# Kernel optimization log

Hardware: AMD Instinct MI355X
Metric: run time of the kernel (lower is better)

Reference implementation:

```python
import jax, jax.numpy as jnp
import numpy as np

EMBED = 256
HEADS = 8
N, L, S = 4, 128, 64


def setup_inputs() -> dict:
    key = jax.random.key(0)
    ks = jax.random.split(key, 9)
    values = jax.random.normal(ks[0], (N, L, S, EMBED), dtype=jnp.float32)
    keys_ = jax.random.normal(ks[1], (N, L, S, EMBED), dtype=jnp.float32)
    query = jax.random.normal(ks[2], (N, L, S, EMBED), dtype=jnp.float32)
    mask = jax.random.randint(ks[3], (N, 1, L, L, 1), 0, 2, dtype=jnp.int32)
    sc = 1.0 / np.sqrt(EMBED)
    Wq = jax.random.normal(ks[4], (EMBED, EMBED), dtype=jnp.float32) * sc
    Wk = jax.random.normal(ks[5], (EMBED, EMBED), dtype=jnp.float32) * sc
    Wv = jax.random.normal(ks[6], (EMBED, EMBED), dtype=jnp.float32) * sc
    Wo = jax.random.normal(ks[7], (HEADS * EMBED, EMBED), dtype=jnp.float32) * (1.0 / np.sqrt(HEADS * EMBED))
    bo = jnp.zeros((EMBED,), dtype=jnp.float32)
    return {"values": values, "keys": keys_, "query": query, "mask": mask,
            "Wq": Wq, "Wk": Wk, "Wv": Wv, "Wo": Wo, "bo": bo}


def reference(values, keys, query, mask, Wq, Wk, Wv, Wo, bo):
    n, q_len, s_len, d = query.shape
    k_len = keys.shape[1]
    h = HEADS
    # Per-head projections share one weight (expand happens BEFORE Linear in
    # the original), so compute each projection once and broadcast over heads.
    q = jnp.einsum('nqsd,de->nqse', query, Wq)   # [N,Q,S,D]
    k = jnp.einsum('nksd,de->nkse', keys, Wk)    # [N,K,S,D]
    v = jnp.einsum('nksd,de->nkse', values, Wv)  # [N,K,S,D]
    # energy: nqshd,nkshd->nhqks ; identical across h pre-mask
    energy = jnp.einsum('nqsd,nksd->nqks', q, k)            # [N,Q,K,S]
    energy = jnp.broadcast_to(energy[:, None], (n, h, q_len, k_len, s_len))
    energy = jnp.where(mask == 0, jnp.float32(-1e20), energy)
    attn = jax.nn.softmax(energy / jnp.sqrt(jnp.float32(d)), axis=3)  # over K
    # out: nhqls,nlshd->nqshd
    out = jnp.einsum('nhqks,nksd->nqshd', attn, v)
    out = out.reshape(n, q_len, s_len, h * d)
    return out @ Wo + bo
```

## Files before the change

### kernel.cpp

```cpp
#include <hip/hip_runtime.h>
#include <hip/hip_bf16.h>


using bf16x4 = __attribute__((ext_vector_type(4))) __bf16;
using bf16x8 = __attribute__((ext_vector_type(8))) __bf16;
using f32x4  = __attribute__((ext_vector_type(4))) float;

#define MFMA(a, b, c) __builtin_amdgcn_mfma_f32_16x16x32_bf16((a), (b), (c), 0, 0, 0)

__global__ __launch_bounds__(256) void prep_pack(
    const float* __restrict__ Wq, const float* __restrict__ Wk,
    const float* __restrict__ Wv, const float* __restrict__ Wo,
    __bf16* __restrict__ wqp, __bf16* __restrict__ wkp,
    __bf16* __restrict__ wvp, __bf16* __restrict__ wop) {
  int idx = blockIdx.x * 256 + threadIdx.x;
  int j = idx & 7, lane = (idx >> 3) & 63, k8 = (idx >> 9) & 7, ct = idx >> 12;
  int e = ct * 16 + (lane & 15);
  int d = k8 * 32 + (lane >> 4) * 8 + j;
  wqp[idx] = (__bf16)Wq[d * 256 + e];
  wkp[idx] = (__bf16)Wk[d * 256 + e];
  wvp[idx] = (__bf16)Wv[d * 256 + e];
  float s = 0.f;
#pragma unroll
  for (int h = 0; h < 8; ++h) s += Wo[(h * 256 + d) * 256 + e];
  wop[idx] = (__bf16)s;
}

__global__ __launch_bounds__(512, 2) void fused_attn(
    const float* __restrict__ Xv, const float* __restrict__ Xk,
    const float* __restrict__ Xq, const int* __restrict__ mask,
    const __bf16* __restrict__ wqp, const __bf16* __restrict__ wkp,
    const __bf16* __restrict__ wvp, const __bf16* __restrict__ wop,
    const float* __restrict__ bo, float* __restrict__ out) {
  extern __shared__ char lds[];
  char* Areg = lds;
  char* Breg = lds + 65536;
  char* Creg = lds + 131072;
  const int t = threadIdx.x, lane = t & 63, w = t >> 6;
  const int lr = lane & 15, g = lane >> 4;
  const int sl = blockIdx.x, n = sl >> 6, s = sl & 63;

  auto fill = [&](const float* __restrict__ X, float4* vr) {
#pragma unroll
    for (int i = 0; i < 8; ++i) {
      int f8 = i * 512 + t, row = f8 >> 5, c8 = f8 & 31;
      const float* src = X + ((size_t)(n * 8192 + row * 64 + s)) * 256 + c8 * 8;
      vr[2 * i]     = *reinterpret_cast<const float4*>(src);
      vr[2 * i + 1] = *reinterpret_cast<const float4*>(src + 4);
    }
  };
  auto flushv = [&](const float4* vr) {
#pragma unroll
    for (int i = 0; i < 8; ++i) {
      int f8 = i * 512 + t, row = f8 >> 5, c8 = f8 & 31;
      bf16x8 b;
      b[0]=(__bf16)vr[2*i].x;   b[1]=(__bf16)vr[2*i].y;
      b[2]=(__bf16)vr[2*i].z;   b[3]=(__bf16)vr[2*i].w;
      b[4]=(__bf16)vr[2*i+1].x; b[5]=(__bf16)vr[2*i+1].y;
      b[6]=(__bf16)vr[2*i+1].z; b[7]=(__bf16)vr[2*i+1].w;
      *reinterpret_cast<bf16x8*>(
          Areg + row * 512 + ((c8 * 16) ^ ((row & 7) << 4))) = b;
    }
  };

  auto projQK = [&](const __bf16* __restrict__ wpk) {
    const bf16x8* wp = reinterpret_cast<const bf16x8*>(wpk);
    bf16x8 wf0[8], wf1[8];
#pragma unroll
    for (int k8 = 0; k8 < 8; ++k8) {
      wf0[k8] = wp[((2 * w)     * 8 + k8) * 64 + lane];
      wf1[k8] = wp[((2 * w + 1) * 8 + k8) * 64 + lane];
    }
#pragma unroll
    for (int ct = 0; ct < 8; ++ct) {
      bf16x8 xf[8];
#pragma unroll
      for (int k8 = 0; k8 < 8; ++k8) {
        int brow = ct * 16 + lr;
        xf[k8] = *reinterpret_cast<const bf16x8*>(
            Areg + brow * 512 + ((k8 * 64 + g * 16) ^ ((brow & 7) << 4)));
      }
      f32x4 a0 = {0.f,0.f,0.f,0.f}, a1 = {0.f,0.f,0.f,0.f};
#pragma unroll
      for (int k8 = 0; k8 < 8; ++k8) {
        a0 = MFMA(wf0[k8], xf[k8], a0);
        a1 = MFMA(wf1[k8], xf[k8], a1);
      }
      bf16x4 p0, p1;
#pragma unroll
      for (int j = 0; j < 4; ++j) { p0[j] = (__bf16)a0[j]; p1[j] = (__bf16)a1[j]; }
      *reinterpret_cast<bf16x4*>(
          Breg + ct * 8192 + w * 1024 + (lr + 16 * (0 + (g >> 1))) * 16 + (g & 1) * 8) = p0;
      *reinterpret_cast<bf16x4*>(
          Breg + ct * 8192 + w * 1024 + (lr + 16 * (2 + (g >> 1))) * 16 + (g & 1) * 8) = p1;
    }
  };

  {
    float4 vr[16];
    fill(Xq, vr);
    flushv(vr);
  }
  __syncthreads();
  float4 vrp[16];
  fill(Xk, vrp);
  projQK(wqp);
  __syncthreads();
  bf16x8 af[8];
#pragma unroll
  for (int k8 = 0; k8 < 8; ++k8)
    af[k8] = *reinterpret_cast<const bf16x8*>(Breg + w * 8192 + k8 * 1024 + lane * 16);
  flushv(vrp);
  __syncthreads();

  fill(Xv, vrp);
  projQK(wkp);
  __syncthreads();

  int mreg[8][4];
#pragma unroll
  for (int ct = 0; ct < 8; ++ct)
#pragma unroll
    for (int j = 0; j < 4; ++j)
      mreg[ct][j] = mask[((size_t)n * 128 + w * 16 + 4 * g + j) * 128 + ct * 16 + lr];
  f32x4 sacc[8];
#pragma unroll
  for (int ct = 0; ct < 8; ++ct) {
    bf16x8 bfr[8];
#pragma unroll
    for (int k8 = 0; k8 < 8; ++k8)
      bfr[k8] = *reinterpret_cast<const bf16x8*>(Breg + ct * 8192 + k8 * 1024 + lane * 16);
    f32x4 a = {0.f,0.f,0.f,0.f};
#pragma unroll
    for (int k8 = 0; k8 < 8; ++k8) a = MFMA(af[k8], bfr[k8], a);
    sacc[ct] = a;
  }
  flushv(vrp);
  __syncthreads();

  float p[8][4];
#pragma unroll
  for (int j = 0; j < 4; ++j) {
    float mx = -3e38f;
#pragma unroll
    for (int ct = 0; ct < 8; ++ct) {
      float sv = mreg[ct][j] ? sacc[ct][j] * 0.0625f : -6.25e18f;
      p[ct][j] = sv;
      mx = fmaxf(mx, sv);
    }
#pragma unroll
    for (int o = 1; o < 16; o <<= 1) mx = fmaxf(mx, __shfl_xor(mx, o));
    float sum = 0.f;
#pragma unroll
    for (int ct = 0; ct < 8; ++ct) {
      float e = __expf(p[ct][j] - mx);
      p[ct][j] = e;
      sum += e;
    }
#pragma unroll
    for (int o = 1; o < 16; o <<= 1) sum += __shfl_xor(sum, o);
    float inv = 1.f / sum;
#pragma unroll
    for (int ct = 0; ct < 8; ++ct) p[ct][j] *= inv;
  }
#pragma unroll
  for (int ct = 0; ct < 8; ++ct) {
    char* bse = Breg + w * 4096 + (ct >> 1) * 1024 +
                (16 * ((ct * 2 + (lr >> 3)) & 3)) * 16 + (lr & 7) * 2;
#pragma unroll
    for (int j = 0; j < 4; ++j)
      *reinterpret_cast<__bf16*>(bse + (4 * g + j) * 16) = (__bf16)p[ct][j];
  }
  bf16x8 pa[4];
#pragma unroll
  for (int kk8 = 0; kk8 < 4; ++kk8)
    pa[kk8] = *reinterpret_cast<const bf16x8*>(Breg + w * 4096 + kk8 * 1024 + lane * 16);

  {
    const bf16x8* wp = reinterpret_cast<const bf16x8*>(wvp);
    bf16x8 vf0[8], vf1[8];
#pragma unroll
    for (int k8 = 0; k8 < 8; ++k8) {
      vf0[k8] = wp[((2 * w)     * 8 + k8) * 64 + lane];
      vf1[k8] = wp[((2 * w + 1) * 8 + k8) * 64 + lane];
    }
#pragma unroll
    for (int half = 0; half < 2; ++half) {
      char* dest = half ? Areg : Creg;
#pragma unroll
      for (int ctl = 0; ctl < 4; ++ctl) {
        int ct = half * 4 + ctl;
        bf16x8 xf[8];
#pragma unroll
        for (int k8 = 0; k8 < 8; ++k8) {
          int brow = ct * 16 + lr;
          xf[k8] = *reinterpret_cast<const bf16x8*>(
              Areg + brow * 512 + ((k8 * 64 + g * 16) ^ ((brow & 7) << 4)));
        }
        f32x4 a0 = {0.f,0.f,0.f,0.f}, a1 = {0.f,0.f,0.f,0.f};
#pragma unroll
        for (int k8 = 0; k8 < 8; ++k8) {
          a0 = MFMA(vf0[k8], xf[k8], a0);
          a1 = MFMA(vf1[k8], xf[k8], a1);
        }
        int kk8loc = (ct >> 1) & 1;
#pragma unroll
        for (int dth = 0; dth < 2; ++dth) {
          const f32x4& ac = dth ? a1 : a0;
          char* bse = dest + ((2 * w + dth) * 2 + kk8loc) * 1024 +
                      (16 * ((ct * 2 + (lr >> 3)) & 3)) * 16 + (lr & 7) * 2;
#pragma unroll
          for (int j = 0; j < 4; ++j)
            *reinterpret_cast<__bf16*>(bse + (4 * g + j) * 16) = (__bf16)ac[j];
        }
      }
      __syncthreads();
    }
  }

#pragma unroll
  for (int dt = 0; dt < 16; ++dt) {
    f32x4 acc = {0.f,0.f,0.f,0.f};
#pragma unroll
    for (int kk8 = 0; kk8 < 4; ++kk8) {
      const char* vb = (kk8 < 2) ? (Creg + (dt * 2 + kk8) * 1024)
                                 : (Areg + (dt * 2 + kk8 - 2) * 1024);
      acc = MFMA(pa[kk8], *reinterpret_cast<const bf16x8*>(vb + lane * 16), acc);
    }
    char* bse = Breg + w * 8192 + (dt >> 1) * 1024 +
                (16 * ((dt * 2 + (lr >> 3)) & 3)) * 16 + (lr & 7) * 2;
#pragma unroll
    for (int j = 0; j < 4; ++j)
      *reinterpret_cast<__bf16*>(bse + (4 * g + j) * 16) = (__bf16)acc[j];
  }
  __syncthreads();

  {
    const bf16x8* wo = reinterpret_cast<const bf16x8*>(wop);
    bf16x8 of0[8], of1[8];
#pragma unroll
    for (int k8 = 0; k8 < 8; ++k8) {
      of0[k8] = wo[((2 * w)     * 8 + k8) * 64 + lane];
      of1[k8] = wo[((2 * w + 1) * 8 + k8) * 64 + lane];
    }
    float4 bias0 = *reinterpret_cast<const float4*>(bo + (2 * w)     * 16 + 4 * g);
    float4 bias1 = *reinterpret_cast<const float4*>(bo + (2 * w + 1) * 16 + 4 * g);
#pragma unroll
    for (int qt = 0; qt < 8; ++qt) {
      bf16x8 bfr[8];
#pragma unroll
      for (int k8 = 0; k8 < 8; ++k8)
        bfr[k8] = *reinterpret_cast<const bf16x8*>(Breg + qt * 8192 + k8 * 1024 + lane * 16);
      f32x4 a0 = {0.f,0.f,0.f,0.f}, a1 = {0.f,0.f,0.f,0.f};
#pragma unroll
      for (int k8 = 0; k8 < 8; ++k8) {
        a0 = MFMA(of0[k8], bfr[k8], a0);
        a1 = MFMA(of1[k8], bfr[k8], a1);
      }
      int q = qt * 16 + lr;
      float* orow = out + ((size_t)n * 8192 + q * 64 + s) * 256;
      float4 o0, o1;
      o0.x = a0[0] + bias0.x; o0.y = a0[1] + bias0.y;
      o0.z = a0[2] + bias0.z; o0.w = a0[3] + bias0.w;
      o1.x = a1[0] + bias1.x; o1.y = a1[1] + bias1.y;
      o1.z = a1[2] + bias1.z; o1.w = a1[3] + bias1.w;
      *reinterpret_cast<float4*>(orow + (2 * w)     * 16 + 4 * g) = o0;
      *reinterpret_cast<float4*>(orow + (2 * w + 1) * 16 + 4 * g) = o1;
    }
  }
}

extern "C" void kernel_launch(void* const* d_in, const int* in_sizes, int n_in,
                              void* d_out, int out_size, void* d_ws, size_t ws_size,
                              hipStream_t stream) {
  const float* values = (const float*)d_in[0];
  const float* keys   = (const float*)d_in[1];
  const float* query  = (const float*)d_in[2];
  const int*   mask   = (const int*)d_in[3];
  const float* Wq     = (const float*)d_in[4];
  const float* Wk     = (const float*)d_in[5];
  const float* Wv     = (const float*)d_in[6];
  const float* Wo     = (const float*)d_in[7];
  const float* bo     = (const float*)d_in[8];
  float* out = (float*)d_out;

  char* w = (char*)d_ws;
  __bf16* wqp = (__bf16*)w; w += 131072;
  __bf16* wkp = (__bf16*)w; w += 131072;
  __bf16* wvp = (__bf16*)w; w += 131072;
  __bf16* wop = (__bf16*)w; w += 131072;

  prep_pack<<<256, 256, 0, stream>>>(Wq, Wk, Wv, Wo, wqp, wkp, wvp, wop);
  fused_attn<<<256, 512, 163840, stream>>>(values, keys, query, mask,
                                           wqp, wkp, wvp, wop, bo, out);
}
```

Before: 47.68 us.

## Fold Wq·Wkᵀ and Wv·Wo_sum into combined weights, dropping K projection and output GEMM

```diff
diff --git a/kernel.cpp b/kernel.cpp
--- a/kernel.cpp
+++ b/kernel.cpp
@@ -8,34 +8,83 @@
 
 #define MFMA(a, b, c) __builtin_amdgcn_mfma_f32_16x16x32_bf16((a), (b), (c), 0, 0, 0)
 
-__global__ __launch_bounds__(256) void prep_pack(
+__device__ __forceinline__ bf16x8 cvt8(float4 f0, float4 f1) {
+  bf16x8 a;
+  a[0]=(__bf16)f0.x; a[1]=(__bf16)f0.y; a[2]=(__bf16)f0.z; a[3]=(__bf16)f0.w;
+  a[4]=(__bf16)f1.x; a[5]=(__bf16)f1.y; a[6]=(__bf16)f1.z; a[7]=(__bf16)f1.w;
+  return a;
+}
+
+__global__ __launch_bounds__(256) void prep_wosum(
+    const float* __restrict__ Wo, float* __restrict__ wosum) {
+  int eo = threadIdx.x, e2 = blockIdx.x;
+  float s = 0.f;
+#pragma unroll
+  for (int h = 0; h < 8; ++h) s += Wo[((size_t)(h * 256 + e2)) * 256 + eo];
+  wosum[e2 * 256 + eo] = s;
+}
+
+__global__ __launch_bounds__(512) void prep_mm(
     const float* __restrict__ Wq, const float* __restrict__ Wk,
-    const float* __restrict__ Wv, const float* __restrict__ Wo,
-    __bf16* __restrict__ wqp, __bf16* __restrict__ wkp,
-    __bf16* __restrict__ wvp, __bf16* __restrict__ wop) {
-  int idx = blockIdx.x * 256 + threadIdx.x;
-  int j = idx & 7, lane = (idx >> 3) & 63, k8 = (idx >> 9) & 7, ct = idx >> 12;
-  int e = ct * 16 + (lane & 15);
-  int d = k8 * 32 + (lane >> 4) * 8 + j;
-  wqp[idx] = (__bf16)Wq[d * 256 + e];
-  wkp[idx] = (__bf16)Wk[d * 256 + e];
-  wvp[idx] = (__bf16)Wv[d * 256 + e];
-  float s = 0.f;
-#pragma unroll
-  for (int h = 0; h < 8; ++h) s += Wo[(h * 256 + d) * 256 + e];
-  wop[idx] = (__bf16)s;
+    const float* __restrict__ Wv, const float* __restrict__ wosum,
+    __bf16* __restrict__ mqk, __bf16* __restrict__ mvo) {
+  const int t = threadIdx.x, lane = t & 63, w = t >> 6;
+  const int lr = lane & 15, g = lane >> 4;
+  const bool isV = blockIdx.y != 0;
+  const float* A = isV ? Wv : Wq;
+  __bf16* dst = isV ? mvo : mqk;
+  bf16x8 af0[8], af1[8];
+#pragma unroll
+  for (int k8 = 0; k8 < 8; ++k8) {
+    const float* p0 = A + (size_t)((2 * w)     * 16 + lr) * 256 + k8 * 32 + g * 8;
+    const float* p1 = A + (size_t)((2 * w + 1) * 16 + lr) * 256 + k8 * 32 + g * 8;
+    af0[k8] = cvt8(*(const float4*)p0, *(const float4*)(p0 + 4));
+    af1[k8] = cvt8(*(const float4*)p1, *(const float4*)(p1 + 4));
+  }
+#pragma unroll
+  for (int c = 0; c < 2; ++c) {
+    int ct = blockIdx.x * 2 + c;
+    bf16x8 bf[8];
+    if (!isV) {
+#pragma unroll
+      for (int k8 = 0; k8 < 8; ++k8) {
+        const float* p = Wk + (size_t)(ct * 16 + lr) * 256 + k8 * 32 + g * 8;
+        bf[k8] = cvt8(*(const float4*)p, *(const float4*)(p + 4));
+      }
+    } else {
+#pragma unroll
+      for (int k8 = 0; k8 < 8; ++k8)
+#pragma unroll
+        for (int jj = 0; jj < 8; ++jj)
+          bf[k8][jj] = (__bf16)wosum[(size_t)(k8 * 32 + g * 8 + jj) * 256 + ct * 16 + lr];
+    }
+    f32x4 a0 = {0.f,0.f,0.f,0.f}, a1 = {0.f,0.f,0.f,0.f};
+#pragma unroll
+    for (int k8 = 0; k8 < 8; ++k8) {
+      a0 = MFMA(af0[k8], bf[k8], a0);
+      a1 = MFMA(af1[k8], bf[k8], a1);
+    }
+#pragma unroll
+    for (int rtl = 0; rtl < 2; ++rtl) {
+      const f32x4& ac = rtl ? a1 : a0;
+      bf16x4 pb;
+#pragma unroll
+      for (int j = 0; j < 4; ++j) pb[j] = (__bf16)ac[j];
+      size_t off = (size_t)ct * 4096 + w * 512 +
+                   ((2 * rtl + (g >> 1)) * 16 + lr) * 8 + 4 * (g & 1);
+      *reinterpret_cast<bf16x4*>(dst + off) = pb;
+    }
+  }
 }
 
 __global__ __launch_bounds__(512, 2) void fused_attn(
     const float* __restrict__ Xv, const float* __restrict__ Xk,
     const float* __restrict__ Xq, const int* __restrict__ mask,
-    const __bf16* __restrict__ wqp, const __bf16* __restrict__ wkp,
-    const __bf16* __restrict__ wvp, const __bf16* __restrict__ wop,
+    const __bf16* __restrict__ mqk, const __bf16* __restrict__ mvo,
     const float* __restrict__ bo, float* __restrict__ out) {
   extern __shared__ char lds[];
   char* Areg = lds;
   char* Breg = lds + 65536;
-  char* Creg = lds + 131072;
   const int t = threadIdx.x, lane = t & 63, w = t >> 6;
   const int lr = lane & 15, g = lane >> 4;
   const int sl = blockIdx.x, n = sl >> 6, s = sl & 63;
@@ -63,8 +112,17 @@
     }
   };
 
-  auto projQK = [&](const __bf16* __restrict__ wpk) {
-    const bf16x8* wp = reinterpret_cast<const bf16x8*>(wpk);
+  {
+    float4 vr[16];
+    fill(Xq, vr);
+    flushv(vr);
+  }
+  __syncthreads();
+
+  float4 vrp[16];
+  fill(Xk, vrp);
+  {
+    const bf16x8* wp = reinterpret_cast<const bf16x8*>(mqk);
     bf16x8 wf0[8], wf1[8];
 #pragma unroll
     for (int k8 = 0; k8 < 8; ++k8) {
@@ -94,18 +152,9 @@
       *reinterpret_cast<bf16x4*>(
           Breg + ct * 8192 + w * 1024 + (lr + 16 * (2 + (g >> 1))) * 16 + (g & 1) * 8) = p1;
     }
-  };
-
-  {
-    float4 vr[16];
-    fill(Xq, vr);
-    flushv(vr);
-  }
-  __syncthreads();
-  float4 vrp[16];
-  fill(Xk, vrp);
-  projQK(wqp);
-  __syncthreads();
+  }
+  __syncthreads();
+
   bf16x8 af[8];
 #pragma unroll
   for (int k8 = 0; k8 < 8; ++k8)
@@ -114,9 +163,6 @@
   __syncthreads();
 
   fill(Xv, vrp);
-  projQK(wkp);
-  __syncthreads();
-
   int mreg[8][4];
 #pragma unroll
   for (int ct = 0; ct < 8; ++ct)
@@ -126,17 +172,20 @@
   f32x4 sacc[8];
 #pragma unroll
   for (int ct = 0; ct < 8; ++ct) {
-    bf16x8 bfr[8];
-#pragma unroll
-    for (int k8 = 0; k8 < 8; ++k8)
-      bfr[k8] = *reinterpret_cast<const bf16x8*>(Breg + ct * 8192 + k8 * 1024 + lane * 16);
+    bf16x8 xf[8];
+#pragma unroll
+    for (int k8 = 0; k8 < 8; ++k8) {
+      int brow = ct * 16 + lr;
+      xf[k8] = *reinterpret_cast<const bf16x8*>(
+          Areg + brow * 512 + ((k8 * 64 + g * 16) ^ ((brow & 7) << 4)));
+    }
     f32x4 a = {0.f,0.f,0.f,0.f};
 #pragma unroll
-    for (int k8 = 0; k8 < 8; ++k8) a = MFMA(af[k8], bfr[k8], a);
+    for (int k8 = 0; k8 < 8; ++k8) a = MFMA(af[k8], xf[k8], a);
     sacc[ct] = a;
   }
+  __syncthreads();
   flushv(vrp);
-  __syncthreads();
 
   float p[8][4];
 #pragma unroll
@@ -175,9 +224,10 @@
 #pragma unroll
   for (int kk8 = 0; kk8 < 4; ++kk8)
     pa[kk8] = *reinterpret_cast<const bf16x8*>(Breg + w * 4096 + kk8 * 1024 + lane * 16);
+  __syncthreads();
 
   {
-    const bf16x8* wp = reinterpret_cast<const bf16x8*>(wvp);
+    const bf16x8* wp = reinterpret_cast<const bf16x8*>(mvo);
     bf16x8 vf0[8], vf1[8];
 #pragma unroll
     for (int k8 = 0; k8 < 8; ++k8) {
@@ -185,87 +235,53 @@
       vf1[k8] = wp[((2 * w + 1) * 8 + k8) * 64 + lane];
     }
 #pragma unroll
-    for (int half = 0; half < 2; ++half) {
-      char* dest = half ? Areg : Creg;
-#pragma unroll
-      for (int ctl = 0; ctl < 4; ++ctl) {
-        int ct = half * 4 + ctl;
-        bf16x8 xf[8];
-#pragma unroll
-        for (int k8 = 0; k8 < 8; ++k8) {
-          int brow = ct * 16 + lr;
-          xf[k8] = *reinterpret_cast<const bf16x8*>(
-              Areg + brow * 512 + ((k8 * 64 + g * 16) ^ ((brow & 7) << 4)));
-        }
-        f32x4 a0 = {0.f,0.f,0.f,0.f}, a1 = {0.f,0.f,0.f,0.f};
-#pragma unroll
-        for (int k8 = 0; k8 < 8; ++k8) {
-          a0 = MFMA(vf0[k8], xf[k8], a0);
-          a1 = MFMA(vf1[k8], xf[k8], a1);
-        }
-        int kk8loc = (ct >> 1) & 1;
-#pragma unroll
-        for (int dth = 0; dth < 2; ++dth) {
-          const f32x4& ac = dth ? a1 : a0;
-          char* bse = dest + ((2 * w + dth) * 2 + kk8loc) * 1024 +
-                      (16 * ((ct * 2 + (lr >> 3)) & 3)) * 16 + (lr & 7) * 2;
-#pragma unroll
-          for (int j = 0; j < 4; ++j)
-            *reinterpret_cast<__bf16*>(bse + (4 * g + j) * 16) = (__bf16)ac[j];
-        }
-      }
-      __syncthreads();
-    }
-  }
-
-#pragma unroll
-  for (int dt = 0; dt < 16; ++dt) {
-    f32x4 acc = {0.f,0.f,0.f,0.f};
-#pragma unroll
-    for (int kk8 = 0; kk8 < 4; ++kk8) {
-      const char* vb = (kk8 < 2) ? (Creg + (dt * 2 + kk8) * 1024)
-                                 : (Areg + (dt * 2 + kk8 - 2) * 1024);
-      acc = MFMA(pa[kk8], *reinterpret_cast<const bf16x8*>(vb + lane * 16), acc);
-    }
-    char* bse = Breg + w * 8192 + (dt >> 1) * 1024 +
-                (16 * ((dt * 2 + (lr >> 3)) & 3)) * 16 + (lr & 7) * 2;
-#pragma unroll
-    for (int j = 0; j < 4; ++j)
-      *reinterpret_cast<__bf16*>(bse + (4 * g + j) * 16) = (__bf16)acc[j];
+    for (int ct = 0; ct < 8; ++ct) {
+      bf16x8 xf[8];
+#pragma unroll
+      for (int k8 = 0; k8 < 8; ++k8) {
+        int brow = ct * 16 + lr;
+        xf[k8] = *reinterpret_cast<const bf16x8*>(
+            Areg + brow * 512 + ((k8 * 64 + g * 16) ^ ((brow & 7) << 4)));
+      }
+      f32x4 a0 = {0.f,0.f,0.f,0.f}, a1 = {0.f,0.f,0.f,0.f};
+#pragma unroll
+      for (int k8 = 0; k8 < 8; ++k8) {
+        a0 = MFMA(vf0[k8], xf[k8], a0);
+        a1 = MFMA(vf1[k8], xf[k8], a1);
+      }
+      int kk8 = ct >> 1;
+#pragma unroll
+      for (int dth = 0; dth < 2; ++dth) {
+        const f32x4& ac = dth ? a1 : a0;
+        char* bse = Breg + ((2 * w + dth) * 4 + kk8) * 1024 +
+                    (16 * ((ct * 2 + (lr >> 3)) & 3)) * 16 + (lr & 7) * 2;
+#pragma unroll
+        for (int j = 0; j < 4; ++j)
+          *reinterpret_cast<__bf16*>(bse + (4 * g + j) * 16) = (__bf16)ac[j];
+      }
+    }
   }
   __syncthreads();
 
   {
-    const bf16x8* wo = reinterpret_cast<const bf16x8*>(wop);
-    bf16x8 of0[8], of1[8];
-#pragma unroll
-    for (int k8 = 0; k8 < 8; ++k8) {
-      of0[k8] = wo[((2 * w)     * 8 + k8) * 64 + lane];
-      of1[k8] = wo[((2 * w + 1) * 8 + k8) * 64 + lane];
-    }
-    float4 bias0 = *reinterpret_cast<const float4*>(bo + (2 * w)     * 16 + 4 * g);
-    float4 bias1 = *reinterpret_cast<const float4*>(bo + (2 * w + 1) * 16 + 4 * g);
-#pragma unroll
-    for (int qt = 0; qt < 8; ++qt) {
-      bf16x8 bfr[8];
-#pragma unroll
-      for (int k8 = 0; k8 < 8; ++k8)
-        bfr[k8] = *reinterpret_cast<const bf16x8*>(Breg + qt * 8192 + k8 * 1024 + lane * 16);
-      f32x4 a0 = {0.f,0.f,0.f,0.f}, a1 = {0.f,0.f,0.f,0.f};
-#pragma unroll
-      for (int k8 = 0; k8 < 8; ++k8) {
-        a0 = MFMA(of0[k8], bfr[k8], a0);
-        a1 = MFMA(of1[k8], bfr[k8], a1);
-      }
-      int q = qt * 16 + lr;
-      float* orow = out + ((size_t)n * 8192 + q * 64 + s) * 256;
-      float4 o0, o1;
-      o0.x = a0[0] + bias0.x; o0.y = a0[1] + bias0.y;
-      o0.z = a0[2] + bias0.z; o0.w = a0[3] + bias0.w;
-      o1.x = a1[0] + bias1.x; o1.y = a1[1] + bias1.y;
-      o1.z = a1[2] + bias1.z; o1.w = a1[3] + bias1.w;
-      *reinterpret_cast<float4*>(orow + (2 * w)     * 16 + 4 * g) = o0;
-      *reinterpret_cast<float4*>(orow + (2 * w + 1) * 16 + 4 * g) = o1;
+    float br[16];
+#pragma unroll
+    for (int et = 0; et < 16; ++et) br[et] = bo[et * 16 + lr];
+#pragma unroll
+    for (int et = 0; et < 16; ++et) {
+      bf16x8 bfr[4];
+#pragma unroll
+      for (int kk8 = 0; kk8 < 4; ++kk8)
+        bfr[kk8] = *reinterpret_cast<const bf16x8*>(
+            Breg + (et * 4 + kk8) * 1024 + lane * 16);
+      f32x4 a = {0.f,0.f,0.f,0.f};
+#pragma unroll
+      for (int kk8 = 0; kk8 < 4; ++kk8) a = MFMA(pa[kk8], bfr[kk8], a);
+#pragma unroll
+      for (int j = 0; j < 4; ++j) {
+        int q = w * 16 + 4 * g + j;
+        out[((size_t)n * 8192 + q * 64 + s) * 256 + et * 16 + lr] = a[j] + br[et];
+      }
     }
   }
 }
@@ -285,12 +301,12 @@
   float* out = (float*)d_out;
 
   char* w = (char*)d_ws;
-  __bf16* wqp = (__bf16*)w; w += 131072;
-  __bf16* wkp = (__bf16*)w; w += 131072;
-  __bf16* wvp = (__bf16*)w; w += 131072;
-  __bf16* wop = (__bf16*)w; w += 131072;
-
-  prep_pack<<<256, 256, 0, stream>>>(Wq, Wk, Wv, Wo, wqp, wkp, wvp, wop);
-  fused_attn<<<256, 512, 163840, stream>>>(values, keys, query, mask,
-                                           wqp, wkp, wvp, wop, bo, out);
-}
+  float*  wosum = (float*)w;  w += 262144;
+  __bf16* mqk   = (__bf16*)w; w += 131072;
+  __bf16* mvo   = (__bf16*)w; w += 131072;
+
+  prep_wosum<<<256, 256, 0, stream>>>(Wo, wosum);
+  prep_mm<<<dim3(8, 2), 512, 0, stream>>>(Wq, Wk, Wv, wosum, mqk, mvo);
+  fused_attn<<<256, 512, 131072, stream>>>(values, keys, query, mask,
+                                           mqk, mvo, bo, out);
+}
```

After: 57.18 us. +19.9%, slower.
